# Kernel optimization log

Hardware: AMD Instinct MI355X
Metric: run time of the kernel (lower is better)

The kernel has to match this reference:

```python
import jax, jax.numpy as jnp
import numpy as np

B, T, D = 4, 8192, 1024
H = 16
HD = D // H  # 64
TOP_K = 64


def setup_inputs() -> dict:
    key = jax.random.key(0)
    ks = jax.random.split(key, 6)
    x = jax.random.normal(ks[0], (B, T, D), dtype=jnp.float32)
    # torch nn.Linear weights are [out, in]; y = x @ W.T
    Wq = jax.random.normal(ks[1], (D, D), dtype=jnp.float32) * 0.02
    Wk = jax.random.normal(ks[2], (D, D), dtype=jnp.float32) * 0.02
    Wv = jax.random.normal(ks[3], (D, D), dtype=jnp.float32) * 0.02
    Wo = jax.random.normal(ks[4], (D, D), dtype=jnp.float32) * 0.02
    # indexer: nn.Linear(head_dim, 1, bias=False) -> weight [1, HD]; keep as [HD]
    w_score = jax.random.normal(ks[5], (HD,), dtype=jnp.float32) * 0.02
    return {"x": x, "Wq": Wq, "Wk": Wk, "Wv": Wv, "Wo": Wo, "w_score": w_score}


def reference(x, Wq, Wk, Wv, Wo, w_score):
    b, t, d = x.shape
    top_k = min(TOP_K, t)
    # projections: [B,T,D] -> [B,H,T,HD]
    def proj(W):
        return jnp.einsum('btd,ed->bte', x, W).reshape(b, t, H, HD).transpose(0, 2, 1, 3)
    q = proj(Wq)
    k = proj(Wk)
    v = proj(Wv)
    # lightning indexer scores: [B,H,T]
    idx_scores = jnp.einsum('bhtd,d->bht', k, w_score)
    _, top_idx = jax.lax.top_k(idx_scores, top_k)  # [B,H,K]
    idx = top_idx[..., None]  # [B,H,K,1]
    k_sparse = jnp.take_along_axis(k, idx, axis=2)  # [B,H,K,HD]
    v_sparse = jnp.take_along_axis(v, idx, axis=2)
    scale = HD ** -0.5
    scores = jnp.einsum('bhtd,bhkd->bhtk', q, k_sparse) * scale  # [B,H,T,K]
    attn = jax.nn.softmax(scores, axis=-1)
    out = jnp.einsum('bhtk,bhkd->bhtd', attn, v_sparse)  # [B,H,T,HD]
    out = out.transpose(0, 2, 1, 3).reshape(b, t, d)
    return jnp.einsum('btd,ed->bte', out, Wo)
```

## Files before the change

kernel.cpp:

```cpp
#include <hip/hip_runtime.h>
#include <hip/hip_bf16.h>
#include <stdint.h>

#define NB 4
#define NT 8192
#define ND 1024
#define NH 16
#define NHD 64
#define NK 64
#define NM (NB*NT)

typedef __attribute__((ext_vector_type(4))) float f32x4;
typedef __attribute__((ext_vector_type(8))) short s16x8;
typedef const void __attribute__((address_space(1)))* gas1_t;
typedef void __attribute__((address_space(3)))* las3_t;

__device__ __forceinline__ float bf2f(ushort u) {
  union { uint32_t i; float f; } v; v.i = ((uint32_t)u) << 16; return v.f;
}
__device__ __forceinline__ ushort f2bf(float f) {
  union { float f; uint32_t i; } v; v.f = f;
  uint32_t r = v.i + 0x7FFFu + ((v.i >> 16) & 1u);
  return (ushort)(r >> 16);
}
__device__ __forceinline__ uint32_t f2ord(uint32_t u) {
  return (u & 0x80000000u) ? ~u : (u | 0x80000000u);
}

__global__ __launch_bounds__(256) void convert_w_kernel(
    const float* __restrict__ Wq, const float* __restrict__ Wk,
    const float* __restrict__ Wv, const float* __restrict__ Wo,
    ushort* __restrict__ wqb, ushort* __restrict__ wkb,
    ushort* __restrict__ wvb, ushort* __restrict__ wob) {
  int i = blockIdx.x * 256 + threadIdx.x;
  wqb[i] = f2bf(Wq[i]); wkb[i] = f2bf(Wk[i]);
  wvb[i] = f2bf(Wv[i]); wob[i] = f2bf(Wo[i]);
}

__global__ __launch_bounds__(256) void prep_u_kernel(
    const float* __restrict__ Wk, const float* __restrict__ wscore,
    float* __restrict__ u) {
  int e = (blockIdx.x & 3) * 256 + threadIdx.x;
  int h = blockIdx.x >> 2;
  float acc = 0.f;
  #pragma unroll 8
  for (int d = 0; d < NHD; ++d) acc += wscore[d] * Wk[(size_t)(h*NHD + d)*ND + e];
  u[h*ND + e] = acc;
}

__global__ __launch_bounds__(256) __attribute__((amdgpu_waves_per_eu(4, 4)))
void prep_x_kernel(
    const float* __restrict__ x, const float* __restrict__ u,
    ushort* __restrict__ xb, float* __restrict__ scores) {
  __shared__ float pbuf[16][4][17];
  int t = threadIdx.x, w = t >> 6, l = t & 63;
  int e0 = w * 256 + l * 4;
  f32x4 uv[16];
  #pragma unroll
  for (int h = 0; h < 16; ++h) uv[h] = *(const f32x4*)(u + h * ND + e0);
  #pragma unroll
  for (int h = 0; h < 16; ++h) asm volatile("" : "+v"(uv[h]));
  __builtin_amdgcn_sched_barrier(0);
  int row0 = blockIdx.x * 32;
  int boff = ((row0 >> 13) << 4);
  int tt0 = row0 & (NT - 1);
  for (int batch = 0; batch < 2; ++batch) {
    #pragma unroll 2
    for (int rr = 0; rr < 16; ++rr) {
      int row = row0 + batch * 16 + rr;
      f32x4 xv = *(const f32x4*)(x + (size_t)row * ND + e0);
      ushort4 o; o.x = f2bf(xv[0]); o.y = f2bf(xv[1]); o.z = f2bf(xv[2]); o.w = f2bf(xv[3]);
      *(ushort4*)(xb + (size_t)row * ND + e0) = o;
      float p[16];
      #pragma unroll
      for (int h = 0; h < 16; ++h)
        p[h] = xv[0]*uv[h][0] + xv[1]*uv[h][1] + xv[2]*uv[h][2] + xv[3]*uv[h][3];
      float q8[8];
      #pragma unroll
      for (int j = 0; j < 8; ++j) {
        bool hi = (l & 1);
        float keep = hi ? p[2*j+1] : p[2*j];
        float send = hi ? p[2*j]   : p[2*j+1];
        q8[j] = keep + __shfl_xor(send, 1, 64);
      }
      float q4[4];
      #pragma unroll
      for (int j = 0; j < 4; ++j) {
        bool hi = ((l >> 1) & 1);
        float keep = hi ? q8[2*j+1] : q8[2*j];
        float send = hi ? q8[2*j]   : q8[2*j+1];
        q4[j] = keep + __shfl_xor(send, 2, 64);
      }
      float q2[2];
      #pragma unroll
      for (int j = 0; j < 2; ++j) {
        bool hi = ((l >> 2) & 1);
        float keep = hi ? q4[2*j+1] : q4[2*j];
        float send = hi ? q4[2*j]   : q4[2*j+1];
        q2[j] = keep + __shfl_xor(send, 4, 64);
      }
      float q1;
      {
        bool hi = ((l >> 3) & 1);
        float keep = hi ? q2[1] : q2[0];
        float send = hi ? q2[0] : q2[1];
        q1 = keep + __shfl_xor(send, 8, 64);
      }
      q1 += __shfl_xor(q1, 16, 64);
      q1 += __shfl_xor(q1, 32, 64);
      if (l < 16) pbuf[rr][w][l] = q1;
    }
    __syncthreads();
    {
      int r16 = t & 15, h = t >> 4;
      float s = pbuf[r16][0][h] + pbuf[r16][1][h] + pbuf[r16][2][h] + pbuf[r16][3][h];
      scores[(size_t)(boff + h) * NT + tt0 + batch * 16 + r16] = s;
    }
    __syncthreads();
  }
}

__global__ __launch_bounds__(256) void topk_kernel(
    const float* __restrict__ scores, int* __restrict__ tidx) {
  int bh = blockIdx.x, t = threadIdx.x;
  __shared__ uint32_t keys[NT];
  __shared__ int hist[4096];
  __shared__ uint32_t ck[512];
  __shared__ int ci[512];
  __shared__ int chunksum[256];
  __shared__ int s_binB, s_c0;
  __shared__ int cnt_hi, cnt_cand;

  for (int i = t; i < 4096; i += 256) hist[i] = 0;
  if (t == 0) { cnt_hi = 0; cnt_cand = 0; }
  __syncthreads();
  const uint4* sg = (const uint4*)(scores + (size_t)bh * NT);
  for (int i = t; i < NT/4; i += 256) {
    uint4 v = sg[i];
    uint32_t k0 = f2ord(v.x), k1 = f2ord(v.y), k2 = f2ord(v.z), k3 = f2ord(v.w);
    keys[i*4+0] = k0; keys[i*4+1] = k1; keys[i*4+2] = k2; keys[i*4+3] = k3;
    atomicAdd(&hist[k0 >> 20], 1); atomicAdd(&hist[k1 >> 20], 1);
    atomicAdd(&hist[k2 >> 20], 1); atomicAdd(&hist[k3 >> 20], 1);
  }
  __syncthreads();
  {
    int hi = 4095 - t * 16;
    int s = 0;
    #pragma unroll
    for (int j = 0; j < 16; ++j) s += hist[hi - j];
    chunksum[t] = s;
  }
  __syncthreads();
  if (t == 0) {
    int cum = 0, c = 0;
    while (cum + chunksum[c] < NK) { cum += chunksum[c]; ++c; }
    int bin = 4095 - c * 16;
    while (cum + hist[bin] < NK) { cum += hist[bin]; --bin; }
    s_binB = bin; s_c0 = cum;
  }
  __syncthreads();
  int binB = s_binB, c0 = s_c0;
  for (int i = t; i < NT; i += 256) {
    int b = keys[i] >> 20;
    if (b > binB) {
      int p = atomicAdd(&cnt_hi, 1);
      tidx[bh*NK + p] = i;
    } else if (b == binB) {
      int p = atomicAdd(&cnt_cand, 1);
      if (p < 512) { ck[p] = keys[i]; ci[p] = i; }
    }
  }
  __syncthreads();
  int nc = cnt_cand; if (nc > 512) nc = 512;
  int need = NK - c0;
  for (int p = t; p < nc; p += 256) {
    uint32_t myk = ck[p]; int myi = ci[p];
    int rank = 0;
    for (int j = 0; j < nc; ++j) {
      uint32_t kj = ck[j];
      rank += (kj > myk || (kj == myk && ci[j] < myi)) ? 1 : 0;
    }
    if (rank < need) tidx[bh*NK + c0 + rank] = myi;
  }
}

__global__ __launch_bounds__(256, 4) void sparse_kv_kernel(
    const ushort* __restrict__ xb, const ushort* __restrict__ wkb,
    const ushort* __restrict__ wvb, const int* __restrict__ tidx,
    ushort* __restrict__ ksp, ushort* __restrict__ vtsp) {
  int bh = blockIdx.x, gy = blockIdx.y;
  int b = bh >> 4, h = bh & 15;
  int t = threadIdx.x;
  __shared__ __align__(16) ushort xl[16][128];
  __shared__ int kid[16];
  if (t < 16) kid[t] = tidx[bh*NK + gy*16 + t];
  int d = t & 63, kq = t >> 6;
  float ak[4] = {0.f,0.f,0.f,0.f}, av[4] = {0.f,0.f,0.f,0.f};
  const ushort* wkr = wkb + (size_t)(h*NHD + d) * ND;
  const ushort* wvr = wvb + (size_t)(h*NHD + d) * ND;
  for (int kc = 0; kc < ND; kc += 128) {
    __syncthreads();
    {
      int row = t >> 4, c8 = (t & 15) * 8;
      *(uint4*)&xl[row][c8] = *(const uint4*)(xb + (size_t)(b*NT + kid[row]) * ND + kc + c8);
    }
    __syncthreads();
    #pragma unroll 1
    for (int sub = 0; sub < 8; ++sub) {
      s16x8 k0 = *(const s16x8*)(wkr + kc + sub*16);
      s16x8 k1 = *(const s16x8*)(wkr + kc + sub*16 + 8);
      s16x8 v0 = *(const s16x8*)(wvr + kc + sub*16);
      s16x8 v1 = *(const s16x8*)(wvr + kc + sub*16 + 8);
      float kf[16], vf2[16];
      #pragma unroll
      for (int j = 0; j < 8; ++j) {
        kf[j]  = bf2f((ushort)k0[j]); kf[8+j]  = bf2f((ushort)k1[j]);
        vf2[j] = bf2f((ushort)v0[j]); vf2[8+j] = bf2f((ushort)v1[j]);
      }
      #pragma unroll
      for (int kk = 0; kk < 4; ++kk) {
        #pragma unroll
        for (int j = 0; j < 16; ++j) {
          float xvv = bf2f(xl[kq*4 + kk][sub*16 + j]);
          ak[kk] += xvv * kf[j];
          av[kk] += xvv * vf2[j];
        }
      }
    }
  }
  #pragma unroll
  for (int kk = 0; kk < 4; ++kk) {
    int key = gy*16 + kq*4 + kk;
    ksp[((size_t)bh*NK + key)*NHD + d] = f2bf(ak[kk]);
    vtsp[((size_t)bh*NHD + d)*NK + key] = f2bf(av[kk]);
  }
}

template<int STORE_BF16>
__global__ __launch_bounds__(512, 2) void gemm8_kernel(
    const ushort* __restrict__ A, const ushort* __restrict__ Bw,
    void* __restrict__ Cout) {
  __shared__ __align__(16) char lds[131072];
  const int t = threadIdx.x, wid = t >> 6, l = t & 63;
  const int wr = wid >> 2, wc = wid & 3;
  int bid = blockIdx.x;
  int wg = (bid & 7) * 64 + (bid >> 3);
  int tm = wg >> 2, tn = wg & 3;
  const int K = 1024, N = 1024;
  const ushort* Ab = A + (size_t)tm * 256 * K;
  const ushort* Bb = Bw + (size_t)tn * 256 * K;
  const int skh  = ((l & 3) * 8) ^ (((l >> 5) & 1) << 4);
  const int srow = l >> 2;
  const int lane_off = (l & 15) * 64 + ((((l >> 4) * 8) ^ (((l >> 3) & 1) << 4)) * 2);
  f32x4 acc[8][4];
  #pragma unroll
  for (int i = 0; i < 8; ++i)
    #pragma unroll
    for (int j = 0; j < 4; ++j) acc[i][j] = (f32x4){0.f, 0.f, 0.f, 0.f};
  s16x8 afr[4][2], bfr[2][2];

#define STG(gbase, matoff, half, ktile, buf) do { \
    const ushort* _s = (gbase) + (size_t)((half)*128 + wid*16 + srow) * K + (ktile)*64 + skh; \
    int _d = (buf)*65536 + (matoff) + ((half)*128 + wid*16)*64; \
    __builtin_amdgcn_global_load_lds((gas1_t)_s, (las3_t)(lds + _d), 16, 0, 0); \
    __builtin_amdgcn_global_load_lds((gas1_t)(_s + 32), (las3_t)(lds + _d + 16384), 16, 0, 0); \
  } while (0)

#define RD_A(mh, kh, buf) do { \
    _Pragma("unroll") \
    for (int mi = 0; mi < 4; ++mi) \
      afr[mi][kh] = *(const s16x8*)(lds + (buf)*65536 + (kh)*16384 + \
                      ((((mh)*2 + wr)*64 + mi*16))*64 + lane_off); \
  } while (0)

#define RD_B(nh, kh, buf) do { \
    _Pragma("unroll") \
    for (int ni = 0; ni < 2; ++ni) \
      bfr[ni][kh] = *(const s16x8*)(lds + (buf)*65536 + 32768 + (kh)*16384 + \
                      (((nh)*128 + wc*32 + ni*16))*64 + lane_off); \
  } while (0)

#define MMAQH(mh, nh, kh) do { \
    __builtin_amdgcn_s_setprio(1); \
    _Pragma("unroll") \
    for (int mi = 0; mi < 4; ++mi) \
      _Pragma("unroll") \
      for (int ni = 0; ni < 2; ++ni) \
        acc[(mh)*4+mi][(nh)*2+ni] = __builtin_amdgcn_mfma_f32_16x16x32_bf16( \
            afr[mi][kh], bfr[ni][kh], acc[(mh)*4+mi][(nh)*2+ni], 0, 0, 0); \
    __builtin_amdgcn_s_setprio(0); \
  } while (0)

#define LG0() do { asm volatile("s_waitcnt lgkmcnt(0)" ::: "memory"); \
                   __builtin_amdgcn_sched_barrier(0); } while (0)
#define ENDPH() do { __builtin_amdgcn_sched_barrier(0); \
                     __builtin_amdgcn_s_barrier(); } while (0)

#define TILE(kt, bc, bn) do { \
  LG0(); MMAQH(0,0,0); RD_A(0,1,bc); RD_B(0,1,bc); ENDPH(); \
  LG0(); MMAQH(0,0,1); RD_B(1,0,bc); \
  if ((kt)+1 < 16) STG(Bb,32768,0,(kt)+1,bn); ENDPH(); \
  LG0(); MMAQH(0,1,0); RD_B(1,1,bc); ENDPH(); \
  LG0(); MMAQH(0,1,1); RD_A(1,0,bc); \
  if ((kt)+2 < 16) STG(Ab,0,0,(kt)+2,bc); ENDPH(); \
  LG0(); MMAQH(1,1,0); RD_A(1,1,bc); ENDPH(); \
  LG0(); MMAQH(1,1,1); RD_B(0,0,bc); \
  if ((kt)+2 < 16) STG(Bb,32768,1,(kt)+2,bc); ENDPH(); \
  LG0(); MMAQH(1,0,0); RD_B(0,1,bc); ENDPH(); \
  LG0(); MMAQH(1,0,1); \
  if ((kt) < 14)       { asm volatile("s_waitcnt vmcnt(4)" ::: "memory"); } \
  else if ((kt) == 14) { asm volatile("s_waitcnt vmcnt(0)" ::: "memory"); } \
  __builtin_amdgcn_sched_barrier(0); \
  __builtin_amdgcn_s_barrier(); \
  if ((kt)+1 < 16) { RD_A(0,0,bn); RD_B(0,0,bn); } \
  if ((kt)+2 < 16) STG(Ab,0,1,(kt)+2,bc); \
} while (0)

  STG(Ab,0,0,0,0); STG(Bb,32768,0,0,0); STG(Ab,0,1,0,0); STG(Bb,32768,1,0,0);
  STG(Ab,0,0,1,1); STG(Bb,32768,1,1,1); STG(Ab,0,1,1,1);
  asm volatile("s_waitcnt vmcnt(6)" ::: "memory");
  __builtin_amdgcn_s_barrier();
  RD_A(0,0,0); RD_B(0,0,0);

  for (int k2 = 0; k2 < 8; ++k2) {
    TILE(2*k2,     0, 1);
    TILE(2*k2 + 1, 1, 0);
  }
#undef TILE
#undef STG
#undef RD_A
#undef RD_B
#undef MMAQH
#undef LG0
#undef ENDPH

  #pragma unroll
  for (int mi8 = 0; mi8 < 8; ++mi8) {
    int grow = tm*256 + (((mi8 >> 2)*2 + wr)*64) + (mi8 & 3)*16 + (l >> 4)*4;
    #pragma unroll
    for (int ni4 = 0; ni4 < 4; ++ni4) {
      int gcol = tn*256 + (ni4 >> 1)*128 + wc*32 + (ni4 & 1)*16 + (l & 15);
      #pragma unroll
      for (int r = 0; r < 4; ++r) {
        size_t off = (size_t)(grow + r) * N + gcol;
        if (STORE_BF16) ((ushort*)Cout)[off] = f2bf(acc[mi8][ni4][r]);
        else            ((float*)Cout)[off]  = acc[mi8][ni4][r];
      }
    }
  }
}

__global__ __launch_bounds__(256, 2) void attn_kernel(
    const ushort* __restrict__ qg, const ushort* __restrict__ ksp,
    const ushort* __restrict__ vtsp, ushort* __restrict__ aout) {
  int bh = blockIdx.y;
  int b = bh >> 4, h = bh & 15;
  int t = threadIdx.x, w = t >> 6, l = t & 63;
  __shared__ __align__(16) ushort Pl[4][1024];
  const ushort* kb = ksp + (size_t)bh * NK * NHD;
  const ushort* vb = vtsp + (size_t)bh * NHD * NK;
  s16x8 kf[2][4], vf[2][4];
  #pragma unroll
  for (int ks = 0; ks < 2; ++ks)
    #pragma unroll
    for (int ni = 0; ni < 4; ++ni) {
      kf[ks][ni] = *(const s16x8*)&kb[(size_t)(ni*16 + (l & 15))*NHD + ks*32 + (l >> 4)*8];
      vf[ks][ni] = *(const s16x8*)&vb[(size_t)(ni*16 + (l & 15))*NK + ks*32 + (l >> 4)*8];
    }
  int rowbase = blockIdx.x * 256 + w * 64;
  #pragma unroll 1
  for (int mi = 0; mi < 4; ++mi) {
    int r0 = rowbase + mi * 16;
    s16x8 af[2];
    #pragma unroll
    for (int ks = 0; ks < 2; ++ks)
      af[ks] = *(const s16x8*)&qg[(size_t)(b*NT + r0 + (l & 15))*ND + h*NHD + ks*32 + (l >> 4)*8];
    f32x4 sc[4];
    #pragma unroll
    for (int ni = 0; ni < 4; ++ni) {
      f32x4 z; z[0]=0.f; z[1]=0.f; z[2]=0.f; z[3]=0.f;
      z = __builtin_amdgcn_mfma_f32_16x16x32_bf16(af[0], kf[0][ni], z, 0, 0, 0);
      sc[ni] = __builtin_amdgcn_mfma_f32_16x16x32_bf16(af[1], kf[1][ni], z, 0, 0, 0);
    }
    #pragma unroll
    for (int r = 0; r < 4; ++r) {
      float v0 = sc[0][r]*0.125f, v1 = sc[1][r]*0.125f;
      float v2 = sc[2][r]*0.125f, v3 = sc[3][r]*0.125f;
      float m = fmaxf(fmaxf(v0, v1), fmaxf(v2, v3));
      #pragma unroll
      for (int mm = 8; mm >= 1; mm >>= 1) m = fmaxf(m, __shfl_xor(m, mm, 64));
      float e0 = __expf(v0 - m), e1 = __expf(v1 - m);
      float e2 = __expf(v2 - m), e3 = __expf(v3 - m);
      float s = e0 + e1 + e2 + e3;
      #pragma unroll
      for (int mm = 8; mm >= 1; mm >>= 1) s += __shfl_xor(s, mm, 64);
      float inv = 1.f / s;
      int prow = (l >> 4)*4 + r;
      int lo = l & 7, hb = (l >> 3) & 1, sw = prow & 7;
      Pl[w][prow*64 + ((0 + hb) ^ sw)*8 + lo] = f2bf(e0 * inv);
      Pl[w][prow*64 + ((2 + hb) ^ sw)*8 + lo] = f2bf(e1 * inv);
      Pl[w][prow*64 + ((4 + hb) ^ sw)*8 + lo] = f2bf(e2 * inv);
      Pl[w][prow*64 + ((6 + hb) ^ sw)*8 + lo] = f2bf(e3 * inv);
    }
    s16x8 pf[2];
    #pragma unroll
    for (int ks = 0; ks < 2; ++ks)
      pf[ks] = *(const s16x8*)&Pl[w][(l & 15)*64 + ((ks*4 + (l >> 4)) ^ (l & 7))*8];
    f32x4 oc[4];
    #pragma unroll
    for (int ni = 0; ni < 4; ++ni) {
      f32x4 z; z[0]=0.f; z[1]=0.f; z[2]=0.f; z[3]=0.f;
      z = __builtin_amdgcn_mfma_f32_16x16x32_bf16(pf[0], vf[0][ni], z, 0, 0, 0);
      oc[ni] = __builtin_amdgcn_mfma_f32_16x16x32_bf16(pf[1], vf[1][ni], z, 0, 0, 0);
    }
    #pragma unroll
    for (int ni = 0; ni < 4; ++ni)
      #pragma unroll
      for (int r = 0; r < 4; ++r) {
        int row = r0 + (l >> 4)*4 + r;
        aout[(size_t)(b*NT + row)*ND + h*NHD + ni*16 + (l & 15)] = f2bf(oc[ni][r]);
      }
  }
}

extern "C" void kernel_launch(void* const* d_in, const int* in_sizes, int n_in,
                              void* d_out, int out_size, void* d_ws, size_t ws_size,
                              hipStream_t stream) {
  (void)in_sizes; (void)n_in; (void)out_size; (void)ws_size;
  const float* x  = (const float*)d_in[0];
  const float* Wq = (const float*)d_in[1];
  const float* Wk = (const float*)d_in[2];
  const float* Wv = (const float*)d_in[3];
  const float* Wo = (const float*)d_in[4];
  const float* wscore = (const float*)d_in[5];

  char* base = (char*)d_ws;
  ushort* xb     = (ushort*)(base + 0);
  ushort* qb     = (ushort*)(base + 67108864);
  float*  scores = (float*) (base + 134217728);
  float*  u      = (float*) (base + 136314880);
  ushort* wqb    = (ushort*)(base + 136380416);
  ushort* wkb    = (ushort*)(base + 138477568);
  ushort* wvb    = (ushort*)(base + 140574720);
  ushort* wob    = (ushort*)(base + 142671872);
  int*    tidx   = (int*)   (base + 144769024);
  ushort* ksp    = (ushort*)(base + 144785408);
  ushort* vtsp   = (ushort*)(base + 145309696);
  ushort* aout   = xb;

  convert_w_kernel<<<dim3(4096), dim3(256), 0, stream>>>(Wq, Wk, Wv, Wo, wqb, wkb, wvb, wob);
  prep_u_kernel<<<dim3(64), dim3(256), 0, stream>>>(Wk, wscore, u);
  prep_x_kernel<<<dim3(1024), dim3(256), 0, stream>>>(x, u, xb, scores);
  topk_kernel<<<dim3(64), dim3(256), 0, stream>>>(scores, tidx);
  sparse_kv_kernel<<<dim3(64, 4), dim3(256), 0, stream>>>(xb, wkb, wvb, tidx, ksp, vtsp);
  gemm8_kernel<1><<<dim3(512), dim3(512), 0, stream>>>(xb, wqb, (void*)qb);
  attn_kernel<<<dim3(32, 64), dim3(256), 0, stream>>>(qb, ksp, vtsp, aout);
  gemm8_kernel<0><<<dim3(512), dim3(512), 0, stream>>>(aout, wob, d_out);
}
```

Before: 295.9 us.

## Split prep_x work across head groups to raise block count and cut registers

The prep_x kernel is split so each block handles 4 of the 16 heads for a 32-row tile, and the grid grows from 1024 to 4096 blocks. Block indices are mapped so the 4 head-group blocks of the same rows sit close together, which should keep re-reads of x in L2. Only the q==0 block writes the bf16 copy of x. This lowers register pressure and shuffle work per block and drops the forced waves_per_eu limit, at the cost of reading x from global memory four times.

```diff
diff --git a/kernel.cpp b/kernel.cpp
--- a/kernel.cpp
+++ b/kernel.cpp
@@ -48,20 +48,22 @@
   u[h*ND + e] = acc;
 }
 
-__global__ __launch_bounds__(256) __attribute__((amdgpu_waves_per_eu(4, 4)))
-void prep_x_kernel(
+__global__ __launch_bounds__(256) void prep_x_kernel(
     const float* __restrict__ x, const float* __restrict__ u,
     ushort* __restrict__ xb, float* __restrict__ scores) {
-  __shared__ float pbuf[16][4][17];
+  __shared__ float pbuf[16][4][5];
   int t = threadIdx.x, w = t >> 6, l = t & 63;
   int e0 = w * 256 + l * 4;
-  f32x4 uv[16];
-  #pragma unroll
-  for (int h = 0; h < 16; ++h) uv[h] = *(const f32x4*)(u + h * ND + e0);
-  #pragma unroll
-  for (int h = 0; h < 16; ++h) asm volatile("" : "+v"(uv[h]));
-  __builtin_amdgcn_sched_barrier(0);
-  int row0 = blockIdx.x * 32;
+  int bid = blockIdx.x;
+  int c = bid & 7, q = (bid >> 3) & 3, a = bid >> 5;
+  int j = a * 8 + c;
+  int q4 = q * 4;
+  f32x4 uv[4];
+  #pragma unroll
+  for (int h = 0; h < 4; ++h) uv[h] = *(const f32x4*)(u + (q4 + h) * ND + e0);
+  #pragma unroll
+  for (int h = 0; h < 4; ++h) asm volatile("" : "+v"(uv[h]));
+  int row0 = j * 32;
   int boff = ((row0 >> 13) << 4);
   int tt0 = row0 & (NT - 1);
   for (int batch = 0; batch < 2; ++batch) {
@@ -69,52 +71,40 @@
     for (int rr = 0; rr < 16; ++rr) {
       int row = row0 + batch * 16 + rr;
       f32x4 xv = *(const f32x4*)(x + (size_t)row * ND + e0);
-      ushort4 o; o.x = f2bf(xv[0]); o.y = f2bf(xv[1]); o.z = f2bf(xv[2]); o.w = f2bf(xv[3]);
-      *(ushort4*)(xb + (size_t)row * ND + e0) = o;
-      float p[16];
-      #pragma unroll
-      for (int h = 0; h < 16; ++h)
+      if (q == 0) {
+        ushort4 o; o.x = f2bf(xv[0]); o.y = f2bf(xv[1]); o.z = f2bf(xv[2]); o.w = f2bf(xv[3]);
+        *(ushort4*)(xb + (size_t)row * ND + e0) = o;
+      }
+      float p[4];
+      #pragma unroll
+      for (int h = 0; h < 4; ++h)
         p[h] = xv[0]*uv[h][0] + xv[1]*uv[h][1] + xv[2]*uv[h][2] + xv[3]*uv[h][3];
-      float q8[8];
-      #pragma unroll
-      for (int j = 0; j < 8; ++j) {
+      float q2[2];
+      #pragma unroll
+      for (int jj = 0; jj < 2; ++jj) {
         bool hi = (l & 1);
-        float keep = hi ? p[2*j+1] : p[2*j];
-        float send = hi ? p[2*j]   : p[2*j+1];
-        q8[j] = keep + __shfl_xor(send, 1, 64);
-      }
-      float q4[4];
-      #pragma unroll
-      for (int j = 0; j < 4; ++j) {
-        bool hi = ((l >> 1) & 1);
-        float keep = hi ? q8[2*j+1] : q8[2*j];
-        float send = hi ? q8[2*j]   : q8[2*j+1];
-        q4[j] = keep + __shfl_xor(send, 2, 64);
-      }
-      float q2[2];
-      #pragma unroll
-      for (int j = 0; j < 2; ++j) {
-        bool hi = ((l >> 2) & 1);
-        float keep = hi ? q4[2*j+1] : q4[2*j];
-        float send = hi ? q4[2*j]   : q4[2*j+1];
-        q2[j] = keep + __shfl_xor(send, 4, 64);
+        float keep = hi ? p[2*jj+1] : p[2*jj];
+        float send = hi ? p[2*jj]   : p[2*jj+1];
+        q2[jj] = keep + __shfl_xor(send, 1, 64);
       }
       float q1;
       {
-        bool hi = ((l >> 3) & 1);
+        bool hi = ((l >> 1) & 1);
         float keep = hi ? q2[1] : q2[0];
         float send = hi ? q2[0] : q2[1];
-        q1 = keep + __shfl_xor(send, 8, 64);
-      }
+        q1 = keep + __shfl_xor(send, 2, 64);
+      }
+      q1 += __shfl_xor(q1, 4, 64);
+      q1 += __shfl_xor(q1, 8, 64);
       q1 += __shfl_xor(q1, 16, 64);
       q1 += __shfl_xor(q1, 32, 64);
-      if (l < 16) pbuf[rr][w][l] = q1;
+      if (l < 4) pbuf[rr][w][l] = q1;
     }
     __syncthreads();
-    {
+    if (t < 64) {
       int r16 = t & 15, h = t >> 4;
       float s = pbuf[r16][0][h] + pbuf[r16][1][h] + pbuf[r16][2][h] + pbuf[r16][3][h];
-      scores[(size_t)(boff + h) * NT + tt0 + batch * 16 + r16] = s;
+      scores[(size_t)(boff + q4 + h) * NT + tt0 + batch * 16 + r16] = s;
     }
     __syncthreads();
   }
@@ -450,7 +440,7 @@
 
   convert_w_kernel<<<dim3(4096), dim3(256), 0, stream>>>(Wq, Wk, Wv, Wo, wqb, wkb, wvb, wob);
   prep_u_kernel<<<dim3(64), dim3(256), 0, stream>>>(Wk, wscore, u);
-  prep_x_kernel<<<dim3(1024), dim3(256), 0, stream>>>(x, u, xb, scores);
+  prep_x_kernel<<<dim3(4096), dim3(256), 0, stream>>>(x, u, xb, scores);
   topk_kernel<<<dim3(64), dim3(256), 0, stream>>>(scores, tidx);
   sparse_kv_kernel<<<dim3(64, 4), dim3(256), 0, stream>>>(xb, wkb, wvb, tidx, ksp, vtsp);
   gemm8_kernel<1><<<dim3(512), dim3(512), 0, stream>>>(xb, wqb, (void*)qb);
```

Result: slower. 318.3 us (+7.6%).
